# Kernel tuning notes

Hardware: AMD Instinct MI355X
Metric: run time of the kernel (lower is better)

Reference implementation:

```python
import jax, jax.numpy as jnp
import numpy as np

B, S, D, H, V, W = 16, 512, 128, 256, 200000, 128

def setup_inputs() -> dict:
    key = jax.random.key(0)
    ks = jax.random.split(key, 12)
    x = jax.random.normal(ks[0], (B, S, D), dtype=jnp.float32)
    word_ids = jax.random.randint(ks[1], (B, S), 0, V)
    raw_len = jax.random.randint(ks[2], (B, S), 1, 5)
    # clamp so t + len - 1 < S (valid scatter targets)
    lengths = jnp.minimum(raw_len, (S - jnp.arange(S))[None, :])
    sc = 0.05
    eye3 = jnp.tile(jnp.eye(H, dtype=jnp.float32), (1, 3))  # paper init for W_hh
    params = dict(
        Wih=jax.random.normal(ks[3], (D, 3 * H), dtype=jnp.float32) * sc,
        Whh=eye3,
        b=jnp.zeros((3 * H,), dtype=jnp.float32),
        aWih=jax.random.normal(ks[4], (D, H), dtype=jnp.float32) * sc,
        aWhh=jnp.eye(H, dtype=jnp.float32),
        ab=jnp.zeros((H,), dtype=jnp.float32),
        wWih=jax.random.normal(ks[5], (W, 3 * H), dtype=jnp.float32) * sc,
        wWhh=eye3,
        wb=jnp.zeros((3 * H,), dtype=jnp.float32),
        emb=jax.random.uniform(ks[6], (V, W), dtype=jnp.float32,
                               minval=-np.sqrt(3.0 / W), maxval=np.sqrt(3.0 / W)),
    )
    return dict(x=x, word_ids=word_ids, lengths=lengths, **params)


def _lattice_scan(x, word_ids, lengths, Wih, Whh, b, aWih, aWhh, ab, wWih, wWhh, wb, emb):
    batch = x.shape[0]
    seq_len = x.shape[1]
    hid = Whh.shape[0]
    xs_t = jnp.transpose(x, (1, 0, 2))        # (S, B, D)
    wid_t = jnp.transpose(word_ids, (1, 0))   # (S, B)
    len_t = jnp.transpose(lengths, (1, 0))    # (S, B)
    ts = jnp.arange(seq_len)
    barange = jnp.arange(batch)

    def step(carry, xt):
        hx, cx, buf = carry
        t, inp, wid, lng = xt
        c_in = buf[t]  # (B, H) skip-word cell state arriving at t
        # MultiInputLSTMCell
        gates = inp @ Wih + hx @ Whh + b              # (B, 3H)
        i, o, g = jnp.split(gates, 3, axis=1)
        i = jax.nn.sigmoid(i)
        o = jax.nn.sigmoid(o)
        g = jnp.tanh(g)
        alpha = jax.nn.sigmoid(inp @ aWih + ab + c_in @ aWhh)  # (B, H)
        # exp of gates, normalized across {i, alpha} (per-element softmax)
        stacked = jnp.stack([i, alpha], axis=1)       # (B, 2, H)
        w = jnp.exp(stacked)
        w = w / w.sum(axis=1, keepdims=True)
        merged = jnp.stack([g, c_in], axis=1)         # (B, 2, H)
        c1 = (merged * w).sum(axis=1)
        h1 = o * jnp.tanh(c1)
        # WordLSTMCell on skip-word embedding (dropout = identity at eval)
        we = emb[wid]                                 # (B, W)
        wg = we @ wWih + h1 @ wWhh + wb               # (B, 3H)
        f, i2, g2 = jnp.split(wg, 3, axis=1)
        ct = jax.nn.sigmoid(f) * c1 + jax.nn.sigmoid(i2) * jnp.tanh(g2)
        # scatter ct to position t + length - 1 per batch element
        buf = buf.at[t + lng - 1, barange].set(ct)
        return (h1, c1, buf), (h1, c1)

    hx0 = jnp.zeros((batch, hid), dtype=x.dtype)
    cx0 = jnp.zeros((batch, hid), dtype=x.dtype)
    buf0 = jnp.zeros((seq_len, batch, hid), dtype=x.dtype)
    _, (h_seq, c_seq) = jax.lax.scan(step, (hx0, cx0, buf0), (ts, xs_t, wid_t, len_t))
    return h_seq, c_seq  # each (S, B, H)


def reference(x, word_ids, lengths, Wih, Whh, b, aWih, aWhh, ab, wWih, wWhh, wb, emb):
    return _lattice_scan(x, word_ids, lengths, Wih, Whh, b, aWih, aWhh, ab, wWih, wWhh, wb, emb)
```

## Files before the change

### kernel.cpp

```cpp
#include <hip/hip_runtime.h>
#include <hip/hip_bf16.h>

#define S_LEN 512
#define B_SZ  16
#define D_IN  128
#define H_HID 256
#define NB    32
#define HSL   8
#define TPB   512

#define L2E   1.44269504088896340736f
#define SNEG  (-1.44269504088896340736f)
#define SPOS2 (2.88539008177792681472f)
#define SN2   (-2.88539008177792681472f)

#define OFF_XP   0
#define OFF_W16  34078720
#define OFF_BSC  34537472
#define OFF_BUF  58720256
#define OFF_HXG  67108864
#define OFF_BAR  67125248

#define XP_SU4   4096

typedef __attribute__((ext_vector_type(4))) float f32x4;
typedef __attribute__((ext_vector_type(8))) short bf16x8;

__device__ __forceinline__ float rcpf(float x){ return __builtin_amdgcn_rcpf(x); }
__device__ __forceinline__ float ex2 (float x){ return __builtin_amdgcn_exp2f(x); }
__device__ __forceinline__ float lg2 (float x){ return __builtin_amdgcn_logf(x); }
__device__ __forceinline__ float U2F(unsigned u){ return __uint_as_float(u); }
__device__ __forceinline__ unsigned bfrne(float f){
  unsigned u = __float_as_uint(f);
  return (u + 0x7FFFu + ((u >> 16) & 1u)) >> 16;
}

__global__ __launch_bounds__(256) void k_prep(const float* __restrict__ Whh,
      const float* __restrict__ aWhh, const float* __restrict__ wWhh,
      const float* __restrict__ Wih, const float* __restrict__ aWih,
      const float* __restrict__ wWihFull,
      const float* __restrict__ bv, const float* __restrict__ abv,
      const float* __restrict__ wbv,
      unsigned short* __restrict__ W16, float* __restrict__ bsc,
      int* __restrict__ flag){
  int t = blockIdx.x*256 + threadIdx.x;
  bool bad = false;
  if (t < 256*768){
    int k = t / 768, c = t - k*768;
    float e = ((c & 255) == k) ? 1.f : 0.f;
    bad = (Whh[t] != e) || (wWhh[t] != e);
  }
  if (t < 65536){
    int k = t >> 8, c = t & 255;
    float e = (c == k) ? 1.f : 0.f;
    bad = bad || (aWhh[t] != e);
  }
  if (bad) atomicOr(flag, 1);
  if (t >= 1792*128) return;
  int k = t / 1792, n = t - k*1792;
  int p = n >> 8, h = n & 255;
  float sc = (p == 2 || p == 6) ? SN2 : SNEG;
  float v;
  if      (p < 3)  v = Wih [k*768 + p*256 + h];
  else if (p == 3) v = aWih[k*256 + h];
  else             v = wWihFull[k*768 + (p-4)*256 + h];
  W16[(size_t)n*128 + k] = (unsigned short)bfrne(v * sc);
  if (k == 0){
    float bb = (p < 3) ? bv[p*256+h] : (p == 3) ? abv[h] : wbv[(p-4)*256+h];
    bsc[n] = bb * sc;
  }
}

__global__ __launch_bounds__(256, 1) void k_pre(const float* __restrict__ x,
      const int* __restrict__ wid, const float* __restrict__ emb,
      const unsigned short* __restrict__ W16, const float* __restrict__ bsc,
      unsigned* __restrict__ xp){
  const int s0 = blockIdx.x*2, tid = threadIdx.x;
  const int wave = tid >> 6, lane = tid & 63;
  __shared__ unsigned short A16[2][2][16][136];
  #pragma unroll
  for (int s2 = 0; s2 < 2; ++s2){
    int s = s0 + s2;
    int b = tid >> 4, k0 = (tid & 15) << 3;
    const float* xs = x + (size_t)(b*S_LEN + s)*D_IN + k0;
    float4 v0 = *(const float4*)xs, v1 = *(const float4*)(xs + 4);
    unsigned short* d = &A16[s2][0][b][k0];
    d[0]=(unsigned short)bfrne(v0.x); d[1]=(unsigned short)bfrne(v0.y);
    d[2]=(unsigned short)bfrne(v0.z); d[3]=(unsigned short)bfrne(v0.w);
    d[4]=(unsigned short)bfrne(v1.x); d[5]=(unsigned short)bfrne(v1.y);
    d[6]=(unsigned short)bfrne(v1.z); d[7]=(unsigned short)bfrne(v1.w);
    long long w = wid[b*S_LEN + s];
    const float* es = emb + w*(long long)D_IN + k0;
    float4 e0 = *(const float4*)es, e1 = *(const float4*)(es + 4);
    d = &A16[s2][1][b][k0];
    d[0]=(unsigned short)bfrne(e0.x); d[1]=(unsigned short)bfrne(e0.y);
    d[2]=(unsigned short)bfrne(e0.z); d[3]=(unsigned short)bfrne(e0.w);
    d[4]=(unsigned short)bfrne(e1.x); d[5]=(unsigned short)bfrne(e1.y);
    d[6]=(unsigned short)bfrne(e1.z); d[7]=(unsigned short)bfrne(e1.w);
  }
  __syncthreads();
  const int lrow = lane & 15, lk = (lane >> 4) << 3;
  bf16x8 afr[2][2][4];
  #pragma unroll
  for (int s2 = 0; s2 < 2; ++s2)
    #pragma unroll
    for (int ks = 0; ks < 4; ++ks){
      afr[s2][0][ks] = *(const bf16x8*)&A16[s2][0][lrow][lk + ks*32];
      afr[s2][1][ks] = *(const bf16x8*)&A16[s2][1][lrow][lk + ks*32];
    }
  #pragma unroll
  for (int g = 0; g < 4; ++g){
    const int hcol = ((wave*4 + g) << 4) + lrow;
    f32x4 acc[2][7];
    #pragma unroll
    for (int p = 0; p < 7; ++p){
      const unsigned short* Wb = W16 + (size_t)(p*256 + hcol)*128 + lk;
      bf16x8 bfr[4];
      #pragma unroll
      for (int ks = 0; ks < 4; ++ks) bfr[ks] = *(const bf16x8*)(Wb + ks*32);
      float bb = bsc[p*256 + hcol];
      #pragma unroll
      for (int s2 = 0; s2 < 2; ++s2){
        f32x4 a = {0.f, 0.f, 0.f, 0.f};
        #pragma unroll
        for (int ks = 0; ks < 4; ++ks)
          a = __builtin_amdgcn_mfma_f32_16x16x32_bf16(afr[s2][p < 4 ? 0 : 1][ks], bfr[ks], a, 0, 0, 0);
        a[0] = ex2(a[0] + bb); a[1] = ex2(a[1] + bb);
        a[2] = ex2(a[2] + bb); a[3] = ex2(a[3] + bb);
        acc[s2][p] = a;
      }
    }
    #pragma unroll
    for (int s2 = 0; s2 < 2; ++s2)
      #pragma unroll
      for (int r = 0; r < 4; ++r){
        unsigned d0 = bfrne(acc[s2][0][r]) | (bfrne(acc[s2][1][r]) << 16);
        unsigned d1 = bfrne(acc[s2][2][r]) | (bfrne(acc[s2][3][r]) << 16);
        unsigned d2 = bfrne(acc[s2][4][r]) | (bfrne(acc[s2][5][r]) << 16);
        unsigned d3 = bfrne(acc[s2][6][r]);
        int row = ((lane >> 4) << 2) + r;
        ((uint4*)xp)[(size_t)((s0+s2)*16 + row)*256 + hcol] = make_uint4(d0, d1, d2, d3);
      }
  }
}

#define DO_STEP(u_, DV_, SL_) {                                               \
  const int us_ = (u_) & 3;                                                   \
  float ci = ringC[us_]; float eC = ringE[us_];                               \
  ringC[us_] = 0.f; ringE[us_] = 1.f;                                         \
  uint4 dv = (DV_);                                                           \
  float Pi_ = U2F(dv.x << 16), Po_ = U2F(dv.x & 0xFFFF0000u);                 \
  float Pg_ = U2F(dv.y << 16), Pa_ = U2F(dv.y & 0xFFFF0000u);                 \
  float Pf_ = U2F(dv.z << 16), P2_ = U2F(dv.z & 0xFFFF0000u);                 \
  float Pw_ = U2F(dv.w << 16);                                                \
  float iv = rcpf(fmaf(Pi_, eH, 1.f));                                        \
  float ov = rcpf(fmaf(Po_, eH, 1.f));                                        \
  float gv = fmaf(2.f, rcpf(fmaf(Pg_, eH*eH, 1.f)), -1.f);                    \
  float av = rcpf(fmaf(Pa_, eC, 1.f));                                        \
  float wi = rcpf(1.f + ex2((av - iv) * L2E));                                \
  float c1 = fmaf(wi, gv - ci, ci);                                           \
  float tc = fmaf(2.f, rcpf(1.f + ex2(c1 * SN2)), -1.f);                      \
  float h1 = ov * tc;                                                         \
  float eHn = ex2(SNEG * h1);                                                 \
  float fv = rcpf(fmaf(Pf_, eHn, 1.f));                                       \
  float i2 = rcpf(fmaf(P2_, eHn, 1.f));                                       \
  float g2 = fmaf(2.f, rcpf(fmaf(Pw_, eHn*eHn, 1.f)), -1.f);                  \
  float ct = fmaf(fv, c1, i2 * g2);                                           \
  float eT = ex2(SNEG * ct);                                                  \
  eH = eHn;                                                                   \
  _Pragma("unroll")                                                           \
  for (int j_ = 0; j_ < 4; ++j_)                                              \
    if ((SL_) == j_){ ringC[j_] = ct; ringE[j_] = eT; }                       \
  *ohp = h1; *ocp = c1; ohp += 4096; ocp += 4096;                             \
}

#define PLOAD(BUF, CH) {                                                      \
  _Pragma("unroll")                                                           \
  for (int u_ = 0; u_ < 8; ++u_)                                              \
    BUF[u_] = gp[(size_t)((CH)*8 + u_)*XP_SU4];                               \
  __builtin_amdgcn_sched_barrier(0);                                          \
}
#define PWRITE(BUF, CH) {                                                     \
  _Pragma("unroll")                                                           \
  for (int u_ = 0; u_ < 8; ++u_)                                              \
    ring[(CH) & 3][u_][pl] = BUF[u_];                                         \
  __builtin_amdgcn_sched_barrier(0);                                          \
}

__global__ __launch_bounds__(128) void k_scan_fast(const uint4* __restrict__ xp,
    const int* __restrict__ lens, const int* __restrict__ flag,
    float* __restrict__ out){
  if (*flag) return;
  const int b    = blockIdx.x >> 2;
  const int quad = blockIdx.x & 3;
  const int tid  = threadIdx.x;
  __shared__ uint4 ring[4][8][64];
  __shared__ __align__(16) int lenS[S_LEN];
  for (int i = tid; i < S_LEN; i += 128){
    int ln = lens[b*S_LEN + i];
    lenS[i] = (ln > 1) ? ((i + ln - 1) & 3) : 4;
  }
  __syncthreads();

  if (tid < 64){
    const int h = quad*64 + tid;
    float* ohp = out + b*256 + h;
    float* ocp = ohp + S_LEN*B_SZ*H_HID;
    const int* lp = lenS;
    float eH = 1.f;
    float ringC[4] = {0.f,0.f,0.f,0.f};
    float ringE[4] = {1.f,1.f,1.f,1.f};
    __syncthreads();
    for (int i = 0; i < 64; ++i){
      uint4 v[8];
      #pragma unroll
      for (int u = 0; u < 8; ++u) v[u] = ring[i & 3][u][tid];
      int4 la = *(const int4*)lp; int4 lb = *(const int4*)(lp + 4); lp += 8;
      DO_STEP(0, v[0], la.x)
      DO_STEP(1, v[1], la.y)
      DO_STEP(2, v[2], la.z)
      DO_STEP(3, v[3], la.w)
      DO_STEP(0, v[4], lb.x)
      DO_STEP(1, v[5], lb.y)
      DO_STEP(2, v[6], lb.z)
      DO_STEP(3, v[7], lb.w)
      __syncthreads();
    }
  } else {
    const int pl = tid - 64;
    const int h  = quad*64 + pl;
    const uint4* gp = xp + (size_t)b*256 + h;
    uint4 A[8], B[8];
    PLOAD(A, 0); PLOAD(B, 1);
    PWRITE(A, 0); PLOAD(A, 2);
    PWRITE(B, 1); PLOAD(B, 3);
    PWRITE(A, 2); PLOAD(A, 4);
    __syncthreads();
    for (int i = 0; i < 64; ++i){
      int j = i + 3;
      if (j < 64){
        if (j & 1){
          PWRITE(B, j);
          if (j + 2 < 64) PLOAD(B, j + 2);
        } else {
          PWRITE(A, j);
          if (j + 2 < 64) PLOAD(A, j + 2);
        }
      }
      __syncthreads();
    }
  }
}

__device__ __forceinline__ float xprd(const unsigned* xp, size_t idx16, int q){
  unsigned d = xp[idx16*4 + (q >> 1)];
  float P = (q & 1) ? U2F(d & 0xFFFF0000u) : U2F(d << 16);
  return lg2(P);
}

__global__ __launch_bounds__(TPB) void k_scan_general(
    const float* __restrict__ Whh, const float* __restrict__ aWhh,
    const float* __restrict__ wWhh, const unsigned* __restrict__ xp,
    const int* __restrict__ lens,
    float* __restrict__ buf, float* __restrict__ hxg,
    int* __restrict__ bar, const int* __restrict__ flag,
    float* __restrict__ out) {
  if (*flag == 0) return;
  __shared__ float WhhT[24][260];
  __shared__ float aWhhT[8][260];
  __shared__ float wWhhT[24][260];
  __shared__ float hxS[16][260];
  __shared__ float cinS[16][260];
  __shared__ float combS[32][17];
  __shared__ float c1S[16][9];

  const int j   = blockIdx.x;
  const int tid = threadIdx.x;
  const int h0  = j*HSL;
  const int cd  = tid >> 4;
  const int bb  = tid & 15;

  for (int i = tid; i < 24*256; i += TPB) {
    int c = i >> 8, k = i & 255;
    int q = c >> 3, hh = c & 7;
    WhhT [c][k] = Whh [k*768 + q*256 + h0 + hh];
    wWhhT[c][k] = wWhh[k*768 + q*256 + h0 + hh];
  }
  for (int i = tid; i < 8*256; i += TPB) {
    int c = i >> 8, k = i & 255;
    aWhhT[c][k] = aWhh[k*256 + h0 + c];
  }
  for (int i = tid; i < 16*260; i += TPB) (&hxS[0][0])[i] = 0.f;
  __syncthreads();

  int phase = 0;
  for (int t = 0; t < S_LEN; ++t) {
    for (int i = tid; i < 16*256; i += TPB) {
      int b = i >> 8, k = i & 255;
      cinS[b][k] = buf[(t*16+b)*256 + k];
    }
    __syncthreads();
    {
      const float* wrow = (cd < 24) ? WhhT[cd] : aWhhT[cd-24];
      const float* xrow = (cd < 24) ? hxS[bb]  : cinS[bb];
      float acc = 0.f;
      #pragma unroll 8
      for (int k = 0; k < 256; k += 4) {
        float4 wv = *(const float4*)(wrow + k);
        float4 xv = *(const float4*)(xrow + k);
        acc = fmaf(wv.x, xv.x, acc); acc = fmaf(wv.y, xv.y, acc);
        acc = fmaf(wv.z, xv.z, acc); acc = fmaf(wv.w, xv.w, acc);
      }
      float pre;
      if (cd < 24) {
        int q = cd >> 3, hh = cd & 7;
        float sc = (q == 2) ? SN2 : SNEG;
        pre = xprd(xp, (size_t)(t*16+bb)*256 + h0 + hh, q) + sc*acc;
      } else {
        pre = xprd(xp, (size_t)(t*16+bb)*256 + h0 + (cd-24), 3) + SNEG*acc;
      }
      combS[cd][bb] = pre;
    }
    __syncthreads();
    if (tid < 128) {
      int b = tid >> 3, hh = tid & 7;
      float iv = rcpf(1.f + ex2(combS[     hh][b]));
      float ov = rcpf(1.f + ex2(combS[ 8 + hh][b]));
      float gv = fmaf(2.f, rcpf(ex2(combS[16 + hh][b]) + 1.f), -1.f);
      float av = rcpf(1.f + ex2(combS[24 + hh][b]));
      float ci = cinS[b][h0 + hh];
      float wi = rcpf(1.f + ex2((av - iv) * L2E));
      float c1 = fmaf(wi, gv - ci, ci);
      float h1 = ov * fmaf(2.f, rcpf(ex2(c1 * SN2) + 1.f), -1.f);
      c1S[b][hh] = c1;
      int hg = h0 + hh;
      hxg[b*256 + hg] = h1;
      out[(t*16+b)*256 + hg] = h1;
      out[S_LEN*B_SZ*H_HID + (t*16+b)*256 + hg] = c1;
    }
    __threadfence();
    __syncthreads();
    ++phase;
    if (tid == 0) {
      __hip_atomic_fetch_add(bar, 1, __ATOMIC_ACQ_REL, __HIP_MEMORY_SCOPE_AGENT);
      while (__hip_atomic_load(bar, __ATOMIC_RELAXED, __HIP_MEMORY_SCOPE_AGENT) < NB*phase) {}
    }
    __syncthreads();
    __threadfence();

    if (t == S_LEN-1) break;

    for (int i = tid; i < 16*256; i += TPB) {
      int b = i >> 8, k = i & 255;
      hxS[b][k] = hxg[b*256 + k];
    }
    __syncthreads();
    if (cd < 24) {
      const float* wrow = wWhhT[cd];
      const float* xrow = hxS[bb];
      float acc = 0.f;
      #pragma unroll 8
      for (int k = 0; k < 256; k += 4) {
        float4 wv = *(const float4*)(wrow + k);
        float4 xv = *(const float4*)(xrow + k);
        acc = fmaf(wv.x, xv.x, acc); acc = fmaf(wv.y, xv.y, acc);
        acc = fmaf(wv.z, xv.z, acc); acc = fmaf(wv.w, xv.w, acc);
      }
      int q = cd >> 3, hh = cd & 7;
      float sc = (q == 2) ? SN2 : SNEG;
      combS[cd][bb] = xprd(xp, (size_t)(t*16+bb)*256 + h0 + hh, 4 + q) + sc*acc;
    }
    __syncthreads();
    if (tid < 128) {
      int b = tid >> 3, hh = tid & 7;
      float fv = rcpf(1.f + ex2(combS[     hh][b]));
      float i2 = rcpf(1.f + ex2(combS[ 8 + hh][b]));
      float g2 = fmaf(2.f, rcpf(ex2(combS[16 + hh][b]) + 1.f), -1.f);
      float ct = fmaf(fv, c1S[b][hh], i2*g2);
      int ln = lens[b*S_LEN + t];
      buf[((t+ln-1)*16 + b)*256 + h0 + hh] = ct;
    }
    __threadfence();
    __syncthreads();
    ++phase;
    if (tid == 0) {
      __hip_atomic_fetch_add(bar, 1, __ATOMIC_ACQ_REL, __HIP_MEMORY_SCOPE_AGENT);
      while (__hip_atomic_load(bar, __ATOMIC_RELAXED, __HIP_MEMORY_SCOPE_AGENT) < NB*phase) {}
    }
    __syncthreads();
    __threadfence();
  }
}

extern "C" void kernel_launch(void* const* d_in, const int* in_sizes, int n_in,
                              void* d_out, int out_size, void* d_ws, size_t ws_size,
                              hipStream_t stream) {
  const float* x    = (const float*)d_in[0];
  const int*   wid  = (const int*)  d_in[1];
  const int*   lens = (const int*)  d_in[2];
  const float* Wih  = (const float*)d_in[3];
  const float* Whh  = (const float*)d_in[4];
  const float* bv   = (const float*)d_in[5];
  const float* aWih = (const float*)d_in[6];
  const float* aWhh = (const float*)d_in[7];
  const float* abv  = (const float*)d_in[8];
  const float* wWih = (const float*)d_in[9];
  const float* wWhh = (const float*)d_in[10];
  const float* wbv  = (const float*)d_in[11];
  const float* emb  = (const float*)d_in[12];

  char* ws = (char*)d_ws;
  unsigned* xp = (unsigned*)(ws + OFF_XP);
  unsigned short* W16 = (unsigned short*)(ws + OFF_W16);
  float* bsc = (float*)(ws + OFF_BSC);
  float* buf = (float*)(ws + OFF_BUF);
  float* hxg = (float*)(ws + OFF_HXG);
  int*   bar = (int*)  (ws + OFF_BAR);
  int*   flg = (int*)  (ws + OFF_BAR + 4);
  float* out = (float*)d_out;

  hipMemsetAsync(buf, 0, 8405248, stream);

  k_prep<<<896, 256, 0, stream>>>(Whh, aWhh, wWhh, Wih, aWih, wWih,
                                  bv, abv, wbv, W16, bsc, flg);
  k_pre<<<256, 256, 0, stream>>>(x, wid, emb, W16, bsc, xp);
  k_scan_fast<<<64, 128, 0, stream>>>((const uint4*)xp, lens, flg, out);
  k_scan_general<<<NB, TPB, 0, stream>>>(Whh, aWhh, wWhh, xp, lens,
                                         buf, hxg, bar, flg, out);
}
```

Measured before the change: 121.8 us.

## Interleave two batch elements per scan thread to hide recurrence latency

Each k_scan_fast block now handles two batch elements, so every compute lane runs two independent recurrences interleaved step by step. The grid shrinks from 64 to 32 blocks. The goal is to fill the latency of the serial dependency chain (transcendentals, rcp) with independent work from the second sequence. The producer loop is also simplified: it loads and immediately writes to LDS two chunks ahead instead of ping-ponging two register buffers, which may expose global load latency right before each barrier. Per-thread register pressure and LDS use double, and half as many CUs are used.

After: 197.9 us. +62.5%, slower.

```diff
diff --git a/kernel.cpp b/kernel.cpp
--- a/kernel.cpp
+++ b/kernel.cpp
@@ -144,18 +144,19 @@
   }
 }
 
-#define DO_STEP(u_, DV_, SL_) {                                               \
+
+#define DO_STEP(u_, DV_, SL_, eH_, rC_, rE_, ohp_, ocp_) {                    \
   const int us_ = (u_) & 3;                                                   \
-  float ci = ringC[us_]; float eC = ringE[us_];                               \
-  ringC[us_] = 0.f; ringE[us_] = 1.f;                                         \
+  float ci = rC_[us_]; float eC = rE_[us_];                                   \
+  rC_[us_] = 0.f; rE_[us_] = 1.f;                                             \
   uint4 dv = (DV_);                                                           \
   float Pi_ = U2F(dv.x << 16), Po_ = U2F(dv.x & 0xFFFF0000u);                 \
   float Pg_ = U2F(dv.y << 16), Pa_ = U2F(dv.y & 0xFFFF0000u);                 \
   float Pf_ = U2F(dv.z << 16), P2_ = U2F(dv.z & 0xFFFF0000u);                 \
   float Pw_ = U2F(dv.w << 16);                                                \
-  float iv = rcpf(fmaf(Pi_, eH, 1.f));                                        \
-  float ov = rcpf(fmaf(Po_, eH, 1.f));                                        \
-  float gv = fmaf(2.f, rcpf(fmaf(Pg_, eH*eH, 1.f)), -1.f);                    \
+  float iv = rcpf(fmaf(Pi_, eH_, 1.f));                                       \
+  float ov = rcpf(fmaf(Po_, eH_, 1.f));                                       \
+  float gv = fmaf(2.f, rcpf(fmaf(Pg_, eH_*eH_, 1.f)), -1.f);                  \
   float av = rcpf(fmaf(Pa_, eC, 1.f));                                        \
   float wi = rcpf(1.f + ex2((av - iv) * L2E));                                \
   float c1 = fmaf(wi, gv - ci, ci);                                           \
@@ -167,23 +168,27 @@
   float g2 = fmaf(2.f, rcpf(fmaf(Pw_, eHn*eHn, 1.f)), -1.f);                  \
   float ct = fmaf(fv, c1, i2 * g2);                                           \
   float eT = ex2(SNEG * ct);                                                  \
-  eH = eHn;                                                                   \
+  eH_ = eHn;                                                                  \
   _Pragma("unroll")                                                           \
   for (int j_ = 0; j_ < 4; ++j_)                                              \
-    if ((SL_) == j_){ ringC[j_] = ct; ringE[j_] = eT; }                       \
-  *ohp = h1; *ocp = c1; ohp += 4096; ocp += 4096;                             \
-}
-
-#define PLOAD(BUF, CH) {                                                      \
+    if ((SL_) == j_){ rC_[j_] = ct; rE_[j_] = eT; }                           \
+  *(ohp_) = h1; *(ocp_) = c1; (ohp_) += 4096; (ocp_) += 4096;                 \
+}
+
+#define PLOAD2(CH) {                                                          \
   _Pragma("unroll")                                                           \
-  for (int u_ = 0; u_ < 8; ++u_)                                              \
-    BUF[u_] = gp[(size_t)((CH)*8 + u_)*XP_SU4];                               \
+  for (int u_ = 0; u_ < 8; ++u_){                                             \
+    A0[u_] = gp0[(size_t)((CH)*8 + u_)*XP_SU4];                               \
+    A1[u_] = gp1[(size_t)((CH)*8 + u_)*XP_SU4];                               \
+  }                                                                           \
   __builtin_amdgcn_sched_barrier(0);                                          \
 }
-#define PWRITE(BUF, CH) {                                                     \
+#define PWRITE2(CH) {                                                         \
   _Pragma("unroll")                                                           \
-  for (int u_ = 0; u_ < 8; ++u_)                                              \
-    ring[(CH) & 3][u_][pl] = BUF[u_];                                         \
+  for (int u_ = 0; u_ < 8; ++u_){                                             \
+    rs[((CH) & 3)*1024 + u_*128     ] = A0[u_];                               \
+    rs[((CH) & 3)*1024 + u_*128 + 64] = A1[u_];                               \
+  }                                                                           \
   __builtin_amdgcn_sched_barrier(0);                                          \
 }
 
@@ -191,62 +196,62 @@
     const int* __restrict__ lens, const int* __restrict__ flag,
     float* __restrict__ out){
   if (*flag) return;
-  const int b    = blockIdx.x >> 2;
+  const int bp   = blockIdx.x >> 2;
   const int quad = blockIdx.x & 3;
   const int tid  = threadIdx.x;
-  __shared__ uint4 ring[4][8][64];
-  __shared__ __align__(16) int lenS[S_LEN];
-  for (int i = tid; i < S_LEN; i += 128){
-    int ln = lens[b*S_LEN + i];
-    lenS[i] = (ln > 1) ? ((i + ln - 1) & 3) : 4;
+  const int b0 = 2*bp, b1 = 2*bp + 1;
+  __shared__ uint4 ring[4*8*2*64];
+  __shared__ __align__(16) int lenSd[2][S_LEN];
+  for (int i = tid; i < 2*S_LEN; i += 128){
+    int bi = i >> 9, t = i & 511;
+    int ln = lens[(b0 + bi)*S_LEN + t];
+    lenSd[bi][t] = (ln > 1) ? ((t + ln - 1) & 3) : 4;
   }
   __syncthreads();
 
   if (tid < 64){
-    const int h = quad*64 + tid;
-    float* ohp = out + b*256 + h;
-    float* ocp = ohp + S_LEN*B_SZ*H_HID;
-    const int* lp = lenS;
-    float eH = 1.f;
-    float ringC[4] = {0.f,0.f,0.f,0.f};
-    float ringE[4] = {1.f,1.f,1.f,1.f};
+    const int lane = tid;
+    const int h = quad*64 + lane;
+    float* ohA = out + b0*256 + h;
+    float* ocA = ohA + S_LEN*B_SZ*H_HID;
+    float* ohB = out + b1*256 + h;
+    float* ocB = ohB + S_LEN*B_SZ*H_HID;
+    const int* lpA = lenSd[0];
+    const int* lpB = lenSd[1];
+    float eHa = 1.f, eHb = 1.f;
+    float rCa[4] = {0.f,0.f,0.f,0.f}, rEa[4] = {1.f,1.f,1.f,1.f};
+    float rCb[4] = {0.f,0.f,0.f,0.f}, rEb[4] = {1.f,1.f,1.f,1.f};
     __syncthreads();
     for (int i = 0; i < 64; ++i){
-      uint4 v[8];
-      #pragma unroll
-      for (int u = 0; u < 8; ++u) v[u] = ring[i & 3][u][tid];
-      int4 la = *(const int4*)lp; int4 lb = *(const int4*)(lp + 4); lp += 8;
-      DO_STEP(0, v[0], la.x)
-      DO_STEP(1, v[1], la.y)
-      DO_STEP(2, v[2], la.z)
-      DO_STEP(3, v[3], la.w)
-      DO_STEP(0, v[4], lb.x)
-      DO_STEP(1, v[5], lb.y)
-      DO_STEP(2, v[6], lb.z)
-      DO_STEP(3, v[7], lb.w)
+      const uint4* rwin = ring + (i & 3)*1024 + lane;
+      int4 lA0 = *(const int4*)lpA; int4 lA1 = *(const int4*)(lpA + 4); lpA += 8;
+      int4 lB0 = *(const int4*)lpB; int4 lB1 = *(const int4*)(lpB + 4); lpB += 8;
+      #define STEP2(u_, sA_, sB_)                                             \
+        { uint4 va = rwin[(u_)*128]; uint4 vb = rwin[(u_)*128 + 64];          \
+          DO_STEP(u_, va, sA_, eHa, rCa, rEa, ohA, ocA)                       \
+          DO_STEP(u_, vb, sB_, eHb, rCb, rEb, ohB, ocB) }
+      STEP2(0, lA0.x, lB0.x)
+      STEP2(1, lA0.y, lB0.y)
+      STEP2(2, lA0.z, lB0.z)
+      STEP2(3, lA0.w, lB0.w)
+      STEP2(4, lA1.x, lB1.x)
+      STEP2(5, lA1.y, lB1.y)
+      STEP2(6, lA1.z, lB1.z)
+      STEP2(7, lA1.w, lB1.w)
+      #undef STEP2
       __syncthreads();
     }
   } else {
     const int pl = tid - 64;
-    const int h  = quad*64 + pl;
-    const uint4* gp = xp + (size_t)b*256 + h;
-    uint4 A[8], B[8];
-    PLOAD(A, 0); PLOAD(B, 1);
-    PWRITE(A, 0); PLOAD(A, 2);
-    PWRITE(B, 1); PLOAD(B, 3);
-    PWRITE(A, 2); PLOAD(A, 4);
-    __syncthreads();
-    for (int i = 0; i < 64; ++i){
-      int j = i + 3;
-      if (j < 64){
-        if (j & 1){
-          PWRITE(B, j);
-          if (j + 2 < 64) PLOAD(B, j + 2);
-        } else {
-          PWRITE(A, j);
-          if (j + 2 < 64) PLOAD(A, j + 2);
-        }
-      }
+    const uint4* gp0 = xp + (size_t)b0*256 + quad*64 + pl;
+    const uint4* gp1 = xp + (size_t)b1*256 + quad*64 + pl;
+    uint4* rs = ring + pl;
+    uint4 A0[8], A1[8];
+    PLOAD2(0) PWRITE2(0)
+    PLOAD2(1) PWRITE2(1)
+    __syncthreads();
+    for (int j = 0; j < 64; ++j){
+      if (j + 2 < 64){ PLOAD2(j + 2) PWRITE2(j + 2) }
       __syncthreads();
     }
   }
@@ -424,7 +429,7 @@
   k_prep<<<896, 256, 0, stream>>>(Whh, aWhh, wWhh, Wih, aWih, wWih,
                                   bv, abv, wbv, W16, bsc, flg);
   k_pre<<<256, 256, 0, stream>>>(x, wid, emb, W16, bsc, xp);
-  k_scan_fast<<<64, 128, 0, stream>>>((const uint4*)xp, lens, flg, out);
+  k_scan_fast<<<32, 128, 0, stream>>>((const uint4*)xp, lens, flg, out);
   k_scan_general<<<NB, TPB, 0, stream>>>(Whh, aWhh, wWhh, xp, lens,
                                          buf, hxg, bar, flg, out);
 }
```

## Fuse input projection and fast scan into one kernel with per-step progress flags

Applied to the files above, without the earlier changes.

Merges the precompute GEMM kernel and the fast recurrent scan kernel into a single launch. 256 producer blocks compute the projected gate inputs per timestep and publish a release flag per step. 64 scan blocks spin-wait on those flags before loading each chunk, so the serial scan can start while later timesteps are still being projected. It removes one launch boundary and overlaps the GEMM with the scan. The cost is spin-waiting, an extra memset of the flags, and reliance on producer and consumer blocks being co-resident. If scan blocks are scheduled before producers and occupy all slots, this could deadlock.

Result: slower. 272.1 us (+123.4%).

```diff
diff --git a/kernel.cpp b/kernel.cpp
--- a/kernel.cpp
+++ b/kernel.cpp
@@ -17,6 +17,7 @@
 #define OFF_XP   0
 #define OFF_W16  34078720
 #define OFF_BSC  34537472
+#define OFF_PROG 34544640
 #define OFF_BUF  58720256
 #define OFF_HXG  67108864
 #define OFF_BAR  67125248
@@ -71,78 +72,6 @@
   }
 }
 
-__global__ __launch_bounds__(256, 1) void k_pre(const float* __restrict__ x,
-      const int* __restrict__ wid, const float* __restrict__ emb,
-      const unsigned short* __restrict__ W16, const float* __restrict__ bsc,
-      unsigned* __restrict__ xp){
-  const int s0 = blockIdx.x*2, tid = threadIdx.x;
-  const int wave = tid >> 6, lane = tid & 63;
-  __shared__ unsigned short A16[2][2][16][136];
-  #pragma unroll
-  for (int s2 = 0; s2 < 2; ++s2){
-    int s = s0 + s2;
-    int b = tid >> 4, k0 = (tid & 15) << 3;
-    const float* xs = x + (size_t)(b*S_LEN + s)*D_IN + k0;
-    float4 v0 = *(const float4*)xs, v1 = *(const float4*)(xs + 4);
-    unsigned short* d = &A16[s2][0][b][k0];
-    d[0]=(unsigned short)bfrne(v0.x); d[1]=(unsigned short)bfrne(v0.y);
-    d[2]=(unsigned short)bfrne(v0.z); d[3]=(unsigned short)bfrne(v0.w);
-    d[4]=(unsigned short)bfrne(v1.x); d[5]=(unsigned short)bfrne(v1.y);
-    d[6]=(unsigned short)bfrne(v1.z); d[7]=(unsigned short)bfrne(v1.w);
-    long long w = wid[b*S_LEN + s];
-    const float* es = emb + w*(long long)D_IN + k0;
-    float4 e0 = *(const float4*)es, e1 = *(const float4*)(es + 4);
-    d = &A16[s2][1][b][k0];
-    d[0]=(unsigned short)bfrne(e0.x); d[1]=(unsigned short)bfrne(e0.y);
-    d[2]=(unsigned short)bfrne(e0.z); d[3]=(unsigned short)bfrne(e0.w);
-    d[4]=(unsigned short)bfrne(e1.x); d[5]=(unsigned short)bfrne(e1.y);
-    d[6]=(unsigned short)bfrne(e1.z); d[7]=(unsigned short)bfrne(e1.w);
-  }
-  __syncthreads();
-  const int lrow = lane & 15, lk = (lane >> 4) << 3;
-  bf16x8 afr[2][2][4];
-  #pragma unroll
-  for (int s2 = 0; s2 < 2; ++s2)
-    #pragma unroll
-    for (int ks = 0; ks < 4; ++ks){
-      afr[s2][0][ks] = *(const bf16x8*)&A16[s2][0][lrow][lk + ks*32];
-      afr[s2][1][ks] = *(const bf16x8*)&A16[s2][1][lrow][lk + ks*32];
-    }
-  #pragma unroll
-  for (int g = 0; g < 4; ++g){
-    const int hcol = ((wave*4 + g) << 4) + lrow;
-    f32x4 acc[2][7];
-    #pragma unroll
-    for (int p = 0; p < 7; ++p){
-      const unsigned short* Wb = W16 + (size_t)(p*256 + hcol)*128 + lk;
-      bf16x8 bfr[4];
-      #pragma unroll
-      for (int ks = 0; ks < 4; ++ks) bfr[ks] = *(const bf16x8*)(Wb + ks*32);
-      float bb = bsc[p*256 + hcol];
-      #pragma unroll
-      for (int s2 = 0; s2 < 2; ++s2){
-        f32x4 a = {0.f, 0.f, 0.f, 0.f};
-        #pragma unroll
-        for (int ks = 0; ks < 4; ++ks)
-          a = __builtin_amdgcn_mfma_f32_16x16x32_bf16(afr[s2][p < 4 ? 0 : 1][ks], bfr[ks], a, 0, 0, 0);
-        a[0] = ex2(a[0] + bb); a[1] = ex2(a[1] + bb);
-        a[2] = ex2(a[2] + bb); a[3] = ex2(a[3] + bb);
-        acc[s2][p] = a;
-      }
-    }
-    #pragma unroll
-    for (int s2 = 0; s2 < 2; ++s2)
-      #pragma unroll
-      for (int r = 0; r < 4; ++r){
-        unsigned d0 = bfrne(acc[s2][0][r]) | (bfrne(acc[s2][1][r]) << 16);
-        unsigned d1 = bfrne(acc[s2][2][r]) | (bfrne(acc[s2][3][r]) << 16);
-        unsigned d2 = bfrne(acc[s2][4][r]) | (bfrne(acc[s2][5][r]) << 16);
-        unsigned d3 = bfrne(acc[s2][6][r]);
-        int row = ((lane >> 4) << 2) + r;
-        ((uint4*)xp)[(size_t)((s0+s2)*16 + row)*256 + hcol] = make_uint4(d0, d1, d2, d3);
-      }
-  }
-}
 
 #define DO_STEP(u_, DV_, SL_) {                                               \
   const int us_ = (u_) & 3;                                                   \
@@ -174,6 +103,13 @@
   *ohp = h1; *ocp = c1; ohp += 4096; ocp += 4096;                             \
 }
 
+#define WAITCH(CH) {                                                          \
+  for (int s_ = (CH)*8; s_ < (CH)*8 + 8; ++s_)                                \
+    while (__hip_atomic_load(prog + s_, __ATOMIC_RELAXED,                     \
+                             __HIP_MEMORY_SCOPE_AGENT) == 0) {}               \
+  __threadfence();                                                            \
+}
+
 #define PLOAD(BUF, CH) {                                                      \
   _Pragma("unroll")                                                           \
   for (int u_ = 0; u_ < 8; ++u_)                                              \
@@ -183,27 +119,105 @@
 #define PWRITE(BUF, CH) {                                                     \
   _Pragma("unroll")                                                           \
   for (int u_ = 0; u_ < 8; ++u_)                                              \
-    ring[(CH) & 3][u_][pl] = BUF[u_];                                         \
+    rs[((CH) & 3)*512 + u_*64] = BUF[u_];                                     \
   __builtin_amdgcn_sched_barrier(0);                                          \
 }
 
-__global__ __launch_bounds__(128) void k_scan_fast(const uint4* __restrict__ xp,
-    const int* __restrict__ lens, const int* __restrict__ flag,
-    float* __restrict__ out){
+__global__ __launch_bounds__(256) void k_main(const float* __restrict__ x,
+      const int* __restrict__ wid, const float* __restrict__ emb,
+      const unsigned short* __restrict__ W16, const float* __restrict__ bsc,
+      unsigned* __restrict__ xp, const int* __restrict__ lens,
+      const int* __restrict__ flag, int* prog, float* __restrict__ out){
+  __shared__ __align__(16) unsigned char smem[34816];
+  const int bid = blockIdx.x, tid = threadIdx.x;
+
+  if (bid < 256){
+    unsigned short* S0 = (unsigned short*)smem;
+    unsigned short* S1 = S0 + 16*136;
+    const int wave = tid >> 6, lane = tid & 63;
+    const int lrow = lane & 15, lk = (lane >> 4) << 3;
+    #pragma unroll
+    for (int pass = 0; pass < 2; ++pass){
+      const int s = bid + pass*256;
+      {
+        int b = tid >> 4, k0 = (tid & 15) << 3;
+        const float* xs = x + (size_t)(b*S_LEN + s)*D_IN + k0;
+        float4 v0 = *(const float4*)xs, v1 = *(const float4*)(xs + 4);
+        unsigned short* d = S0 + b*136 + k0;
+        d[0]=(unsigned short)bfrne(v0.x); d[1]=(unsigned short)bfrne(v0.y);
+        d[2]=(unsigned short)bfrne(v0.z); d[3]=(unsigned short)bfrne(v0.w);
+        d[4]=(unsigned short)bfrne(v1.x); d[5]=(unsigned short)bfrne(v1.y);
+        d[6]=(unsigned short)bfrne(v1.z); d[7]=(unsigned short)bfrne(v1.w);
+        long long w = wid[b*S_LEN + s];
+        const float* es = emb + w*(long long)D_IN + k0;
+        float4 e0 = *(const float4*)es, e1 = *(const float4*)(es + 4);
+        d = S1 + b*136 + k0;
+        d[0]=(unsigned short)bfrne(e0.x); d[1]=(unsigned short)bfrne(e0.y);
+        d[2]=(unsigned short)bfrne(e0.z); d[3]=(unsigned short)bfrne(e0.w);
+        d[4]=(unsigned short)bfrne(e1.x); d[5]=(unsigned short)bfrne(e1.y);
+        d[6]=(unsigned short)bfrne(e1.z); d[7]=(unsigned short)bfrne(e1.w);
+      }
+      __syncthreads();
+      bf16x8 afr[2][4];
+      #pragma unroll
+      for (int ks = 0; ks < 4; ++ks){
+        afr[0][ks] = *(const bf16x8*)(S0 + lrow*136 + lk + ks*32);
+        afr[1][ks] = *(const bf16x8*)(S1 + lrow*136 + lk + ks*32);
+      }
+      #pragma unroll
+      for (int g = 0; g < 4; ++g){
+        const int hcol = ((wave*4 + g) << 4) + lrow;
+        f32x4 acc[7];
+        #pragma unroll
+        for (int p = 0; p < 7; ++p){
+          const unsigned short* Wb = W16 + (size_t)(p*256 + hcol)*128 + lk;
+          bf16x8 bfr[4];
+          #pragma unroll
+          for (int ks = 0; ks < 4; ++ks) bfr[ks] = *(const bf16x8*)(Wb + ks*32);
+          float bb = bsc[p*256 + hcol];
+          f32x4 a = {0.f, 0.f, 0.f, 0.f};
+          #pragma unroll
+          for (int ks = 0; ks < 4; ++ks)
+            a = __builtin_amdgcn_mfma_f32_16x16x32_bf16(afr[p < 4 ? 0 : 1][ks], bfr[ks], a, 0, 0, 0);
+          a[0] = ex2(a[0] + bb); a[1] = ex2(a[1] + bb);
+          a[2] = ex2(a[2] + bb); a[3] = ex2(a[3] + bb);
+          acc[p] = a;
+        }
+        #pragma unroll
+        for (int r = 0; r < 4; ++r){
+          unsigned d0 = bfrne(acc[0][r]) | (bfrne(acc[1][r]) << 16);
+          unsigned d1 = bfrne(acc[2][r]) | (bfrne(acc[3][r]) << 16);
+          unsigned d2 = bfrne(acc[4][r]) | (bfrne(acc[5][r]) << 16);
+          unsigned d3 = bfrne(acc[6][r]);
+          int row = ((lane >> 4) << 2) + r;
+          ((uint4*)xp)[(size_t)(s*16 + row)*256 + hcol] = make_uint4(d0, d1, d2, d3);
+        }
+      }
+      __syncthreads();
+      if (tid == 0){
+        __threadfence();
+        __hip_atomic_store(prog + s, 1, __ATOMIC_RELEASE, __HIP_MEMORY_SCOPE_AGENT);
+      }
+    }
+    return;
+  }
+
   if (*flag) return;
-  const int b    = blockIdx.x >> 2;
-  const int quad = blockIdx.x & 3;
-  const int tid  = threadIdx.x;
-  __shared__ uint4 ring[4][8][64];
-  __shared__ __align__(16) int lenS[S_LEN];
-  for (int i = tid; i < S_LEN; i += 128){
+  const int sid  = bid - 256;
+  const int b    = sid >> 2;
+  const int quad = sid & 3;
+  uint4* ring = (uint4*)smem;
+  int*   lenS = (int*)(smem + 32768);
+  for (int i = tid; i < S_LEN; i += 256){
     int ln = lens[b*S_LEN + i];
     lenS[i] = (ln > 1) ? ((i + ln - 1) & 3) : 4;
   }
   __syncthreads();
 
-  if (tid < 64){
-    const int h = quad*64 + tid;
+  const int w = tid >> 6;
+  if (w == 0){
+    const int lane = tid;
+    const int h = quad*64 + lane;
     float* ohp = out + b*256 + h;
     float* ocp = ohp + S_LEN*B_SZ*H_HID;
     const int* lp = lenS;
@@ -212,9 +226,10 @@
     float ringE[4] = {1.f,1.f,1.f,1.f};
     __syncthreads();
     for (int i = 0; i < 64; ++i){
+      const uint4* rw = ring + (i & 3)*512 + lane;
       uint4 v[8];
       #pragma unroll
-      for (int u = 0; u < 8; ++u) v[u] = ring[i & 3][u][tid];
+      for (int u = 0; u < 8; ++u) v[u] = rw[u*64];
       int4 la = *(const int4*)lp; int4 lb = *(const int4*)(lp + 4); lp += 8;
       DO_STEP(0, v[0], la.x)
       DO_STEP(1, v[1], la.y)
@@ -226,29 +241,32 @@
       DO_STEP(3, v[7], lb.w)
       __syncthreads();
     }
-  } else {
+  } else if (w == 1){
     const int pl = tid - 64;
     const int h  = quad*64 + pl;
-    const uint4* gp = xp + (size_t)b*256 + h;
+    const uint4* gp = (const uint4*)xp + (size_t)b*256 + h;
+    uint4* rs = ring + pl;
     uint4 A[8], B[8];
-    PLOAD(A, 0); PLOAD(B, 1);
-    PWRITE(A, 0); PLOAD(A, 2);
-    PWRITE(B, 1); PLOAD(B, 3);
-    PWRITE(A, 2); PLOAD(A, 4);
+    WAITCH(0) PLOAD(A, 0); WAITCH(1) PLOAD(B, 1);
+    PWRITE(A, 0); WAITCH(2) PLOAD(A, 2);
+    PWRITE(B, 1); WAITCH(3) PLOAD(B, 3);
+    PWRITE(A, 2); WAITCH(4) PLOAD(A, 4);
     __syncthreads();
     for (int i = 0; i < 64; ++i){
       int j = i + 3;
       if (j < 64){
         if (j & 1){
           PWRITE(B, j);
-          if (j + 2 < 64) PLOAD(B, j + 2);
+          if (j + 2 < 64){ WAITCH(j + 2) PLOAD(B, j + 2); }
         } else {
           PWRITE(A, j);
-          if (j + 2 < 64) PLOAD(A, j + 2);
+          if (j + 2 < 64){ WAITCH(j + 2) PLOAD(A, j + 2); }
         }
       }
       __syncthreads();
     }
+  } else {
+    for (int i = 0; i < 65; ++i) __syncthreads();
   }
 }
 
@@ -413,6 +431,7 @@
   unsigned* xp = (unsigned*)(ws + OFF_XP);
   unsigned short* W16 = (unsigned short*)(ws + OFF_W16);
   float* bsc = (float*)(ws + OFF_BSC);
+  int*  prog = (int*)  (ws + OFF_PROG);
   float* buf = (float*)(ws + OFF_BUF);
   float* hxg = (float*)(ws + OFF_HXG);
   int*   bar = (int*)  (ws + OFF_BAR);
@@ -420,11 +439,12 @@
   float* out = (float*)d_out;
 
   hipMemsetAsync(buf, 0, 8405248, stream);
+  hipMemsetAsync(prog, 0, S_LEN*sizeof(int), stream);
 
   k_prep<<<896, 256, 0, stream>>>(Whh, aWhh, wWhh, Wih, aWih, wWih,
                                   bv, abv, wbv, W16, bsc, flg);
-  k_pre<<<256, 256, 0, stream>>>(x, wid, emb, W16, bsc, xp);
-  k_scan_fast<<<64, 128, 0, stream>>>((const uint4*)xp, lens, flg, out);
+  k_main<<<320, 256, 0, stream>>>(x, wid, emb, W16, bsc, xp, lens, flg,
+                                  prog, out);
   k_scan_general<<<NB, TPB, 0, stream>>>(Whh, aWhh, wWhh, xp, lens,
                                          buf, hxg, bar, flg, out);
 }
```
